# Kernel optimization log

Measured on AMD Instinct MI355X. Metric: run time of the kernel, lower is better.

## Reference

```python
import jax, jax.numpy as jnp
import numpy as np

B, L, D = 2, 2048, 2048
NH, NKV = 16, 8
HD = D // NH            # 128
GQ = NH // NKV          # queries per kv head
THETA = 10000.0
SCALE = HD ** -0.5


def rope_tables(seq_len, dim, theta):
    inv_freq = 1.0 / theta ** (jnp.arange(0, dim, 2, dtype=jnp.float32) / dim)
    t = jnp.arange(seq_len, dtype=jnp.float32)
    freqs = jnp.outer(t, inv_freq)              # [L, dim/2]
    emb = jnp.concatenate([freqs, freqs], -1)   # [L, dim]
    return jnp.cos(emb), jnp.sin(emb)


def rotate_half(x):
    x1, x2 = jnp.split(x, 2, axis=-1)
    return jnp.concatenate([-x2, x1], -1)


def setup_inputs() -> dict:
    key = jax.random.key(0)
    ks = jax.random.split(key, 5)
    s = 0.02
    return {
        "x": jax.random.normal(ks[0], (B, L, D), jnp.float32),
        "Wq": jax.random.normal(ks[1], (NH * HD, D), jnp.float32) * s,
        "Wk": jax.random.normal(ks[2], (NKV * HD, D), jnp.float32) * s,
        "Wv": jax.random.normal(ks[3], (NKV * HD, D), jnp.float32) * s,
        "Wo": jax.random.normal(ks[4], (D, D), jnp.float32) * s,
    }


def reference(x, Wq, Wk, Wv, Wo):
    b, l, d = x.shape
    q = (x @ Wq.T).reshape(b, l, NH, HD).transpose(0, 2, 1, 3)    # [B,NH,L,HD]
    k = (x @ Wk.T).reshape(b, l, NKV, HD).transpose(0, 2, 1, 3)   # [B,NKV,L,HD]
    v = (x @ Wv.T).reshape(b, l, NKV, HD).transpose(0, 2, 1, 3)

    cos, sin = rope_tables(l, HD, THETA)                           # [L,HD]
    q = q * cos + rotate_half(q) * sin
    k = k * cos + rotate_half(k) * sin

    # GQA without materializing expanded K/V: group queries per kv head
    qg = q.reshape(b, NKV, GQ, l, HD)
    scores = jnp.einsum('bgrld,bgmd->bgrlm', qg, k) * SCALE        # [B,NKV,GQ,L,L]
    causal = jnp.triu(jnp.ones((l, l), bool), k=1)
    scores = jnp.where(causal, -jnp.inf, scores)
    attn = jax.nn.softmax(scores.astype(jnp.float32), axis=-1).astype(q.dtype)
    out = jnp.einsum('bgrlm,bgmd->bgrld', attn, v)                 # [B,NKV,GQ,L,HD]
    out = out.reshape(b, NH, l, HD).transpose(0, 2, 1, 3).reshape(b, l, d)
    return out @ Wo.T
```

## Files before the change

kernel.cpp:

```cpp
#include <hip/hip_runtime.h>
#include <cmath>

using u16 = unsigned short;
typedef u16    u16x4  __attribute__((ext_vector_type(4)));
typedef u16    u16x8  __attribute__((ext_vector_type(8)));
typedef __bf16 bf16x8 __attribute__((ext_vector_type(8)));
typedef float  f32x4  __attribute__((ext_vector_type(4)));

constexpr int Bc  = 2;
constexpr int Lc  = 2048;
constexpr int Dc  = 2048;
constexpr int NHc = 16;
constexpr int NKVc= 8;
constexpr int HDc = 128;

__device__ __forceinline__ u16 f2b(float f) {
  union { float f; unsigned u; } v; v.f = f;
  unsigned r = v.u + 0x7FFFu + ((v.u >> 16) & 1u);
  return (u16)(r >> 16);
}
__device__ __forceinline__ u16 f2b_fast(float f) {
  union { float f; unsigned u; } v; v.f = f;
  return (u16)((v.u + 0x8000u) >> 16);
}
__device__ __forceinline__ float b2f(u16 s) {
  union { unsigned u; float f; } v; v.u = ((unsigned)s) << 16;
  return v.f;
}
__device__ __forceinline__ bf16x8 ld_frag(const u16* p) {
  u16x8 u = *(const u16x8*)p;
  return __builtin_bit_cast(bf16x8, u);
}
__device__ __forceinline__ void gld_lds16(u16* ldst, const u16* gsrc) {
  __builtin_amdgcn_global_load_lds(
      (const __attribute__((address_space(1))) void*)gsrc,
      (__attribute__((address_space(3))) void*)ldst, 16, 0, 0);
}

__global__ void cvt_f32_bf16(const float* __restrict__ src, u16* __restrict__ dst, int n) {
  int i = (blockIdx.x * blockDim.x + threadIdx.x) * 4;
  if (i >= n) return;
  float4 v = *(const float4*)&src[i];
  u16x4 o = { f2b(v.x), f2b(v.y), f2b(v.z), f2b(v.w) };
  *(u16x4*)&dst[i] = o;
}

template <int MODE>
__global__ __launch_bounds__(256) void gemm_lds(
    const u16* __restrict__ A, const u16* __restrict__ W,
    float* __restrict__ Cf, u16* __restrict__ Qp, u16* __restrict__ Kp, u16* __restrict__ Vtp,
    int M, int N, int K)
{
  __shared__ u16 lds[16384];
  u16* lA = lds;
  u16* lB = lds + 8192;
  const int tid  = threadIdx.x;
  const int wave = tid >> 6, lane = tid & 63;
  const int quad = lane >> 4, l16 = lane & 15;
  const int t7   = l16 & 7;
  const int m0 = blockIdx.y * 128, n0 = blockIdx.x * 128;
  const int mw = (wave >> 1) * 64, nw = (wave & 1) * 64;
  const int r8 = lane >> 3;
  const int cgl = (lane & 7) ^ r8;

  f32x4 acc[4][4];
#pragma unroll
  for (int i = 0; i < 4; ++i)
#pragma unroll
    for (int j = 0; j < 4; ++j) acc[i][j] = {0.f, 0.f, 0.f, 0.f};

  for (int kt = 0; kt < K; kt += 64) {
#pragma unroll
    for (int cc = 0; cc < 4; ++cc) {
      int c = wave + cc * 4;
      gld_lds16(&lA[c * 512], &A[(size_t)(m0 + 8 * c + r8) * K + kt + cgl * 8]);
      gld_lds16(&lB[c * 512], &W[(size_t)(n0 + 8 * c + r8) * K + kt + cgl * 8]);
    }
    __syncthreads();
#pragma unroll
    for (int s = 0; s < 2; ++s) {
      bf16x8 af[4], bf[4];
#pragma unroll
      for (int i = 0; i < 4; ++i)
        af[i] = ld_frag(&lA[(mw + i*16 + l16) * 64 + ((quad + 4*s) ^ t7) * 8]);
#pragma unroll
      for (int j = 0; j < 4; ++j)
        bf[j] = ld_frag(&lB[(nw + j*16 + l16) * 64 + ((quad + 4*s) ^ t7) * 8]);
#pragma unroll
      for (int i = 0; i < 4; ++i)
#pragma unroll
        for (int j = 0; j < 4; ++j)
          acc[i][j] = __builtin_amdgcn_mfma_f32_16x16x32_bf16(af[i], bf[j], acc[i][j], 0, 0, 0);
    }
    __syncthreads();
  }

  if constexpr (MODE == 1) {
#pragma unroll
    for (int i = 0; i < 4; ++i)
#pragma unroll
      for (int j = 0; j < 4; ++j)
#pragma unroll
        for (int r = 0; r < 4; ++r) {
          int m = m0 + mw + i*16 + quad*4 + r;
          int n = n0 + nw + j*16 + l16;
          Cf[(size_t)m * N + n] = acc[i][j][r];
        }
  } else {
    if (n0 < 3072) {
      u16* Cb; int ldc, nc0;
      if (n0 < 2048) { Cb = Qp; ldc = 2048; nc0 = n0; }
      else           { Cb = Kp; ldc = 1024; nc0 = n0 - 2048; }
#pragma unroll
      for (int i = 0; i < 4; ++i)
#pragma unroll
        for (int j = 0; j < 4; ++j)
#pragma unroll
          for (int r = 0; r < 4; ++r) {
            int m = m0 + mw + i*16 + quad*4 + r;
            int n = nc0 + nw + j*16 + l16;
            Cb[(size_t)m * ldc + n] = f2b(acc[i][j][r]);
          }
    } else {
#pragma unroll
      for (int i = 0; i < 4; ++i)
#pragma unroll
        for (int j = 0; j < 4; ++j)
#pragma unroll
          for (int r = 0; r < 4; ++r) {
            int l = mw + i*16 + quad*4 + r;
            int d = nw + j*16 + l16;
            int dp = d ^ (((l >> 3) & 15) << 3);
            lds[l * 128 + dp] = f2b(acc[i][j][r]);
          }
      __syncthreads();
      const int b   = m0 >> 11;
      const int hkv = (n0 - 3072) >> 7;
      const size_t vbase = (((size_t)b * NKVc + hkv) * HDc) * (size_t)Lc;
#pragma unroll
      for (int it = 0; it < 8; ++it) {
        int slot = tid + it * 256;
        int d  = slot & 127;
        int l8 = slot >> 7;
        u16x8 v;
#pragma unroll
        for (int e = 0; e < 8; ++e) {
          int l = l8 * 8 + e;
          v[e] = lds[l * 128 + (d ^ (((l >> 3) & 15) << 3))];
        }
        *(u16x8*)&Vtp[vbase + (size_t)d * Lc + (m0 & (Lc - 1)) + l8 * 8] = v;
      }
    }
  }
}

__global__ void rope_kernel(u16* __restrict__ T, int nheads, float oscale)
{
  int idx = blockIdx.x * blockDim.x + threadIdx.x;
  int total = Bc * Lc * nheads * 64;
  if (idx >= total) return;
  int d   = idx & 63;
  int h   = (idx >> 6) % nheads;
  int row = idx / (nheads * 64);
  int l   = row & (Lc - 1);
  float freq = exp2f((float)d * (-13.287712379549449f / 64.f));
  float ang  = (float)l * freq;
  float s, c;
  sincosf(ang, &s, &c);
  size_t base = (size_t)row * (nheads * 128) + h * 128;
  float x1 = b2f(T[base + d]);
  float x2 = b2f(T[base + d + 64]);
  T[base + d]      = f2b((x1 * c - x2 * s) * oscale);
  T[base + d + 64] = f2b((x2 * c + x1 * s) * oscale);
}

__global__ __launch_bounds__(256) void flash_kernel(
    const u16* __restrict__ Q, const u16* __restrict__ K, const u16* __restrict__ Vt,
    u16* __restrict__ O)
{
  __shared__ u16 smem[37376];
  const int tid  = threadIdx.x;
  const int wave = tid >> 6, lane = tid & 63;
  const int quad = lane >> 4, l16 = lane & 15;
  const int bh = blockIdx.x;
  const int b = bh >> 4, h = bh & 15, hkv = h >> 1;

  const size_t kbase = ((size_t)b * Lc) * (NKVc * HDc) + (size_t)hkv * HDc;
  const size_t vbase = (((size_t)b * NKVc + hkv) * HDc) * (size_t)Lc;

  const int kr8  = lane >> 4;
  const int kcl  = lane & 15;
  const int vr16 = lane >> 3;
  const int vkl  = lane & 7;

  u16* sP_w = smem + 32768 + wave * 1152;

  for (int pass = 0; pass < 2; ++pass) {
    const int qt = (pass == 0) ? (31 - (int)blockIdx.y) : (int)blockIdx.y;
    const int q0 = qt * 64;
    const size_t qbase = ((size_t)(b * Lc + q0)) * Dc + (size_t)h * HDc;

    __syncthreads();
    {
      u16* sQ = smem + 24576;
#pragma unroll
      for (int i = 0; i < 4; ++i) {
        int g = tid + i * 256;
        int row = g >> 4, cg = g & 15;
        *(u16x8*)&sQ[row * 128 + (cg ^ (row & 15)) * 8] =
            *(const u16x8*)&Q[qbase + (size_t)row * Dc + cg * 8];
      }
      __syncthreads();
      bf16x8 qf0 = ld_frag(&sQ[(wave*16 + l16) * 128 + ((0*4 + quad) ^ l16) * 8]);
      bf16x8 qf1 = ld_frag(&sQ[(wave*16 + l16) * 128 + ((1*4 + quad) ^ l16) * 8]);
      bf16x8 qf2 = ld_frag(&sQ[(wave*16 + l16) * 128 + ((2*4 + quad) ^ l16) * 8]);
      bf16x8 qf3 = ld_frag(&sQ[(wave*16 + l16) * 128 + ((3*4 + quad) ^ l16) * 8]);
      bf16x8 qf[4] = { qf0, qf1, qf2, qf3 };

#pragma unroll
      for (int cc = 0; cc < 4; ++cc) {
        int c = wave + cc * 4;
        int row = c * 4 + kr8;
        gld_lds16(smem + c * 512,
                  &K[kbase + (size_t)row * (NKVc*HDc) + (size_t)(kcl ^ (row & 15)) * 8]);
      }
#pragma unroll
      for (int cc = 0; cc < 4; ++cc) {
        int c = wave + cc * 4;
        int d = c * 8 + vr16;
        gld_lds16(smem + 16384 + c * 512,
                  &Vt[vbase + (size_t)d * Lc + (size_t)(vkl ^ (d & 7)) * 8]);
      }

      f32x4 acc_o[8];
#pragma unroll
      for (int i = 0; i < 8; ++i) acc_o[i] = {0.f, 0.f, 0.f, 0.f};
      float ps[4] = {0.f, 0.f, 0.f, 0.f};

      for (int kt = 0; kt <= qt; ++kt) {
        const int kOff  = (kt & 1) ? 8192 : 0;
        const int kOffN = (kt & 1) ? 0 : 8192;
        const int vOff  = 16384 + ((kt & 1) ? 8192 : 0);
        const int vOffN = 16384 + ((kt & 1) ? 0 : 8192);

        __asm__ volatile("s_waitcnt vmcnt(4)\n\ts_barrier" ::: "memory");

        if (kt < qt) {
#pragma unroll
          for (int cc = 0; cc < 4; ++cc) {
            int c = wave + cc * 4;
            int row = (kt + 1) * 64 + c * 4 + kr8;
            gld_lds16(smem + kOffN + c * 512,
                      &K[kbase + (size_t)row * (NKVc*HDc) + (size_t)(kcl ^ (row & 15)) * 8]);
          }
        }

        const u16* sKc = smem + kOff;
        f32x4 accs[4];
#pragma unroll
        for (int n = 0; n < 4; ++n) accs[n] = {0.f, 0.f, 0.f, 0.f};
#pragma unroll
        for (int ks = 0; ks < 4; ++ks)
#pragma unroll
          for (int n = 0; n < 4; ++n) {
            bf16x8 kf = ld_frag(&sKc[(n*16 + l16) * 128 + ((ks*4 + quad) ^ l16) * 8]);
            accs[n] = __builtin_amdgcn_mfma_f32_16x16x32_bf16(qf[ks], kf, accs[n], 0, 0, 0);
          }

        const int qrow = q0 + wave*16 + quad*4;
        if (kt == qt) {
#pragma unroll
          for (int n = 0; n < 4; ++n) {
            int kg = kt*64 + n*16 + l16;
#pragma unroll
            for (int r = 0; r < 4; ++r)
              if (kg > qrow + r) accs[n][r] = -INFINITY;
          }
        }
#pragma unroll
        for (int n = 0; n < 4; ++n)
#pragma unroll
          for (int r = 0; r < 4; ++r) {
            float p = exp2f(accs[n][r]);
            accs[n][r] = p;
            ps[r] += p;
          }

#pragma unroll
        for (int n = 0; n < 4; ++n)
#pragma unroll
          for (int r = 0; r < 4; ++r)
            sP_w[(quad*4 + r) * 72 + n*16 + l16] = f2b_fast(accs[n][r]);

        if (kt < qt)
          __asm__ volatile("s_waitcnt vmcnt(4) lgkmcnt(0)\n\ts_barrier" ::: "memory");
        else
          __asm__ volatile("s_waitcnt vmcnt(0) lgkmcnt(0)\n\ts_barrier" ::: "memory");

        if (kt < qt) {
#pragma unroll
          for (int cc = 0; cc < 4; ++cc) {
            int c = wave + cc * 4;
            int d = c * 8 + vr16;
            gld_lds16(smem + vOffN + c * 512,
                      &Vt[vbase + (size_t)d * Lc + (kt+1)*64 + (size_t)(vkl ^ (d & 7)) * 8]);
          }
        }

        const u16* sVc = smem + vOff;
#pragma unroll
        for (int s2 = 0; s2 < 2; ++s2) {
          bf16x8 pf = ld_frag(&sP_w[l16 * 72 + s2*32 + quad*8]);
#pragma unroll
          for (int di = 0; di < 8; ++di) {
            bf16x8 vf = ld_frag(&sVc[(di*16 + l16) * 64 + ((s2*4 + quad) ^ (l16 & 7)) * 8]);
            acc_o[di] = __builtin_amdgcn_mfma_f32_16x16x32_bf16(pf, vf, acc_o[di], 0, 0, 0);
          }
        }
      }

#pragma unroll
      for (int off = 1; off < 16; off <<= 1)
#pragma unroll
        for (int r = 0; r < 4; ++r) ps[r] += __shfl_xor(ps[r], off);
      float inv[4];
#pragma unroll
      for (int r = 0; r < 4; ++r) inv[r] = 1.0f / ps[r];

#pragma unroll
      for (int di = 0; di < 8; ++di)
#pragma unroll
        for (int r = 0; r < 4; ++r) {
          int qrow = q0 + wave*16 + quad*4 + r;
          int d = di*16 + l16;
          float v = acc_o[di][r] * inv[r];
          O[((size_t)(b * Lc + qrow)) * Dc + (size_t)h * HDc + d] = f2b(v);
        }
    }
  }
}

extern "C" void kernel_launch(void* const* d_in, const int* in_sizes, int n_in,
                              void* d_out, int out_size, void* d_ws, size_t ws_size,
                              hipStream_t stream)
{
  const float* x  = (const float*)d_in[0];
  const float* Wq = (const float*)d_in[1];
  const float* Wk = (const float*)d_in[2];
  const float* Wv = (const float*)d_in[3];
  const float* Wo = (const float*)d_in[4];
  float* out = (float*)d_out;

  const int M = Bc * Lc;
  u16* ws = (u16*)d_ws;
  u16* xb   = ws;
  u16* Ow   = xb;
  u16* Wcat = ws + (size_t)8 * 1024 * 1024;
  u16* Wob  = Wcat;
  u16* Qw   = Wcat + (size_t)8 * 1024 * 1024;
  u16* Kw   = Qw   + (size_t)8 * 1024 * 1024;
  u16* Vt   = Kw   + (size_t)4 * 1024 * 1024;

  const int nx = M * Dc;
  const int nq = Dc * Dc;
  const int nk = (NKVc*HDc) * Dc;
  cvt_f32_bf16<<<nx/1024, 256, 0, stream>>>(x,  xb, nx);
  cvt_f32_bf16<<<nq/1024, 256, 0, stream>>>(Wq, Wcat, nq);
  cvt_f32_bf16<<<nk/1024, 256, 0, stream>>>(Wk, Wcat + (size_t)2048*2048, nk);
  cvt_f32_bf16<<<nk/1024, 256, 0, stream>>>(Wv, Wcat + (size_t)3072*2048, nk);

  gemm_lds<2><<<dim3(32, 32), 256, 0, stream>>>(xb, Wcat, nullptr, Qw, Kw, Vt, M, 4096, Dc);

  const float qs = 0.08838834764831845f * 1.4426950408889634f;
  rope_kernel<<<(M * NHc  * 64 + 255) / 256, 256, 0, stream>>>(Qw, NHc,  qs);
  rope_kernel<<<(M * NKVc * 64 + 255) / 256, 256, 0, stream>>>(Kw, NKVc, 1.0f);

  flash_kernel<<<dim3(Bc*NHc, 16), 256, 0, stream>>>(Qw, Kw, Vt, Ow);

  cvt_f32_bf16<<<nq/1024, 256, 0, stream>>>(Wo, Wob, nq);
  gemm_lds<1><<<dim3(16, 32), 256, 0, stream>>>(Ow, Wob, out, nullptr, nullptr, nullptr, M, Dc, Dc);
}
```

Baseline: 345.5 us.

## Share K/V tiles across GQA query heads in flash kernel, merge small launches

The flash kernel now launches one 512-thread block per (batch, kv head) and processes both query heads of that GQA group together. Each K/V tile is loaded into LDS once and used by 8 waves instead of 4, which halves K/V global traffic and the number of blocks. The three weight conversions are merged into one kernel, and the two RoPE launches into one, to cut launch overhead. The trade-offs are fewer blocks in flight (256 instead of 512), a larger LDS footprint, and barriers that now synchronise 8 waves.

```diff
diff --git a/kernel.cpp b/kernel.cpp
--- a/kernel.cpp
+++ b/kernel.cpp
@@ -41,6 +41,22 @@
   int i = (blockIdx.x * blockDim.x + threadIdx.x) * 4;
   if (i >= n) return;
   float4 v = *(const float4*)&src[i];
+  u16x4 o = { f2b(v.x), f2b(v.y), f2b(v.z), f2b(v.w) };
+  *(u16x4*)&dst[i] = o;
+}
+
+__global__ void cvt_w3(const float* __restrict__ Wq, const float* __restrict__ Wk,
+                       const float* __restrict__ Wv, u16* __restrict__ dst) {
+  const int n1 = Dc * Dc;
+  const int n2 = n1 + (NKVc*HDc) * Dc;
+  const int n3 = n2 + (NKVc*HDc) * Dc;
+  int i = (blockIdx.x * blockDim.x + threadIdx.x) * 4;
+  if (i >= n3) return;
+  const float* src; int off;
+  if (i < n1)      { src = Wq; off = i; }
+  else if (i < n2) { src = Wk; off = i - n1; }
+  else             { src = Wv; off = i - n2; }
+  float4 v = *(const float4*)&src[off];
   u16x4 o = { f2b(v.x), f2b(v.y), f2b(v.z), f2b(v.w) };
   *(u16x4*)&dst[i] = o;
 }
@@ -154,11 +170,15 @@
   }
 }
 
-__global__ void rope_kernel(u16* __restrict__ T, int nheads, float oscale)
+__global__ void rope2_kernel(u16* __restrict__ Qp, u16* __restrict__ Kp, float qs)
 {
-  int idx = blockIdx.x * blockDim.x + threadIdx.x;
-  int total = Bc * Lc * nheads * 64;
-  if (idx >= total) return;
+  const int nQ = Bc * Lc * NHc * 64;
+  const int nT = nQ + Bc * Lc * NKVc * 64;
+  int t = blockIdx.x * blockDim.x + threadIdx.x;
+  if (t >= nT) return;
+  u16* T; int nheads; float osc; int idx;
+  if (t < nQ) { T = Qp; nheads = NHc;  osc = qs;  idx = t; }
+  else        { T = Kp; nheads = NKVc; osc = 1.f; idx = t - nQ; }
   int d   = idx & 63;
   int h   = (idx >> 6) % nheads;
   int row = idx / (nheads * 64);
@@ -170,26 +190,28 @@
   size_t base = (size_t)row * (nheads * 128) + h * 128;
   float x1 = b2f(T[base + d]);
   float x2 = b2f(T[base + d + 64]);
-  T[base + d]      = f2b((x1 * c - x2 * s) * oscale);
-  T[base + d + 64] = f2b((x2 * c + x1 * s) * oscale);
-}
-
-__global__ __launch_bounds__(256) void flash_kernel(
+  T[base + d]      = f2b((x1 * c - x2 * s) * osc);
+  T[base + d + 64] = f2b((x2 * c + x1 * s) * osc);
+}
+
+__global__ __launch_bounds__(512) void flash_kernel(
     const u16* __restrict__ Q, const u16* __restrict__ K, const u16* __restrict__ Vt,
     u16* __restrict__ O)
 {
-  __shared__ u16 smem[37376];
+  __shared__ u16 smem[41984];
   const int tid  = threadIdx.x;
   const int wave = tid >> 6, lane = tid & 63;
   const int quad = lane >> 4, l16 = lane & 15;
-  const int bh = blockIdx.x;
-  const int b = bh >> 4, h = bh & 15, hkv = h >> 1;
+  const int hw = wave >> 2, wr = wave & 3;
+  const int bhkv = blockIdx.x;
+  const int b = bhkv >> 3, hkv = bhkv & 7;
+  const int h = hkv * 2 + hw;
 
   const size_t kbase = ((size_t)b * Lc) * (NKVc * HDc) + (size_t)hkv * HDc;
   const size_t vbase = (((size_t)b * NKVc + hkv) * HDc) * (size_t)Lc;
 
-  const int kr8  = lane >> 4;
-  const int kcl  = lane & 15;
+  const int kr8 = lane >> 4;
+  const int kcl = lane & 15;
   const int vr16 = lane >> 3;
   const int vkl  = lane & 7;
 
@@ -198,145 +220,143 @@
   for (int pass = 0; pass < 2; ++pass) {
     const int qt = (pass == 0) ? (31 - (int)blockIdx.y) : (int)blockIdx.y;
     const int q0 = qt * 64;
-    const size_t qbase = ((size_t)(b * Lc + q0)) * Dc + (size_t)h * HDc;
 
     __syncthreads();
-    {
-      u16* sQ = smem + 24576;
-#pragma unroll
-      for (int i = 0; i < 4; ++i) {
-        int g = tid + i * 256;
-        int row = g >> 4, cg = g & 15;
-        *(u16x8*)&sQ[row * 128 + (cg ^ (row & 15)) * 8] =
-            *(const u16x8*)&Q[qbase + (size_t)row * Dc + cg * 8];
-      }
-      __syncthreads();
-      bf16x8 qf0 = ld_frag(&sQ[(wave*16 + l16) * 128 + ((0*4 + quad) ^ l16) * 8]);
-      bf16x8 qf1 = ld_frag(&sQ[(wave*16 + l16) * 128 + ((1*4 + quad) ^ l16) * 8]);
-      bf16x8 qf2 = ld_frag(&sQ[(wave*16 + l16) * 128 + ((2*4 + quad) ^ l16) * 8]);
-      bf16x8 qf3 = ld_frag(&sQ[(wave*16 + l16) * 128 + ((3*4 + quad) ^ l16) * 8]);
-      bf16x8 qf[4] = { qf0, qf1, qf2, qf3 };
-
-#pragma unroll
-      for (int cc = 0; cc < 4; ++cc) {
-        int c = wave + cc * 4;
-        int row = c * 4 + kr8;
-        gld_lds16(smem + c * 512,
-                  &K[kbase + (size_t)row * (NKVc*HDc) + (size_t)(kcl ^ (row & 15)) * 8]);
-      }
-#pragma unroll
-      for (int cc = 0; cc < 4; ++cc) {
-        int c = wave + cc * 4;
-        int d = c * 8 + vr16;
-        gld_lds16(smem + 16384 + c * 512,
-                  &Vt[vbase + (size_t)d * Lc + (size_t)(vkl ^ (d & 7)) * 8]);
-      }
-
-      f32x4 acc_o[8];
-#pragma unroll
-      for (int i = 0; i < 8; ++i) acc_o[i] = {0.f, 0.f, 0.f, 0.f};
-      float ps[4] = {0.f, 0.f, 0.f, 0.f};
-
-      for (int kt = 0; kt <= qt; ++kt) {
-        const int kOff  = (kt & 1) ? 8192 : 0;
-        const int kOffN = (kt & 1) ? 0 : 8192;
-        const int vOff  = 16384 + ((kt & 1) ? 8192 : 0);
-        const int vOffN = 16384 + ((kt & 1) ? 0 : 8192);
-
-        __asm__ volatile("s_waitcnt vmcnt(4)\n\ts_barrier" ::: "memory");
-
-        if (kt < qt) {
-#pragma unroll
-          for (int cc = 0; cc < 4; ++cc) {
-            int c = wave + cc * 4;
-            int row = (kt + 1) * 64 + c * 4 + kr8;
-            gld_lds16(smem + kOffN + c * 512,
-                      &K[kbase + (size_t)row * (NKVc*HDc) + (size_t)(kcl ^ (row & 15)) * 8]);
-          }
-        }
-
-        const u16* sKc = smem + kOff;
-        f32x4 accs[4];
-#pragma unroll
-        for (int n = 0; n < 4; ++n) accs[n] = {0.f, 0.f, 0.f, 0.f};
-#pragma unroll
-        for (int ks = 0; ks < 4; ++ks)
-#pragma unroll
-          for (int n = 0; n < 4; ++n) {
-            bf16x8 kf = ld_frag(&sKc[(n*16 + l16) * 128 + ((ks*4 + quad) ^ l16) * 8]);
-            accs[n] = __builtin_amdgcn_mfma_f32_16x16x32_bf16(qf[ks], kf, accs[n], 0, 0, 0);
-          }
-
-        const int qrow = q0 + wave*16 + quad*4;
-        if (kt == qt) {
-#pragma unroll
-          for (int n = 0; n < 4; ++n) {
-            int kg = kt*64 + n*16 + l16;
-#pragma unroll
-            for (int r = 0; r < 4; ++r)
-              if (kg > qrow + r) accs[n][r] = -INFINITY;
-          }
-        }
-#pragma unroll
-        for (int n = 0; n < 4; ++n)
-#pragma unroll
-          for (int r = 0; r < 4; ++r) {
-            float p = exp2f(accs[n][r]);
-            accs[n][r] = p;
-            ps[r] += p;
-          }
-
-#pragma unroll
-        for (int n = 0; n < 4; ++n)
+#pragma unroll
+    for (int i = 0; i < 4; ++i) {
+      int g = tid + i * 512;
+      int row = g >> 4, cg = g & 15;
+      int qh = hkv * 2 + (row >> 6);
+      int rr = row & 63;
+      *(u16x8*)&smem[row * 128 + (cg ^ (row & 15)) * 8] =
+          *(const u16x8*)&Q[((size_t)(b * Lc + q0 + rr)) * Dc + (size_t)qh * HDc + cg * 8];
+    }
+    __syncthreads();
+    bf16x8 qf[4];
+#pragma unroll
+    for (int ks = 0; ks < 4; ++ks)
+      qf[ks] = ld_frag(&smem[(hw*64 + wr*16 + l16) * 128 + ((ks*4 + quad) ^ l16) * 8]);
+    __syncthreads();
+
+#pragma unroll
+    for (int i = 0; i < 2; ++i) {
+      int c = wave + i * 8;
+      int row = c * 4 + kr8;
+      gld_lds16(smem + c * 512,
+                &K[kbase + (size_t)row * (NKVc*HDc) + (size_t)(kcl ^ (row & 15)) * 8]);
+    }
+#pragma unroll
+    for (int i = 0; i < 2; ++i) {
+      int c = wave + i * 8;
+      int d = c * 8 + vr16;
+      gld_lds16(smem + 16384 + c * 512,
+                &Vt[vbase + (size_t)d * Lc + (size_t)(vkl ^ (d & 7)) * 8]);
+    }
+
+    f32x4 acc_o[8];
+#pragma unroll
+    for (int i = 0; i < 8; ++i) acc_o[i] = {0.f, 0.f, 0.f, 0.f};
+    float ps[4] = {0.f, 0.f, 0.f, 0.f};
+
+    for (int kt = 0; kt <= qt; ++kt) {
+      const int kOff  = (kt & 1) ? 8192 : 0;
+      const int kOffN = (kt & 1) ? 0 : 8192;
+      const int vOff  = (kt & 1) ? 24576 : 16384;
+      const int vOffN = (kt & 1) ? 16384 : 24576;
+
+      __asm__ volatile("s_waitcnt vmcnt(2)\n\ts_barrier" ::: "memory");
+
+      if (kt < qt) {
+#pragma unroll
+        for (int i = 0; i < 2; ++i) {
+          int c = wave + i * 8;
+          int row = (kt + 1) * 64 + c * 4 + kr8;
+          gld_lds16(smem + kOffN + c * 512,
+                    &K[kbase + (size_t)row * (NKVc*HDc) + (size_t)(kcl ^ (row & 15)) * 8]);
+        }
+      }
+
+      const u16* sKc = smem + kOff;
+      f32x4 accs[4];
+#pragma unroll
+      for (int n = 0; n < 4; ++n) accs[n] = {0.f, 0.f, 0.f, 0.f};
+#pragma unroll
+      for (int ks = 0; ks < 4; ++ks)
+#pragma unroll
+        for (int n = 0; n < 4; ++n) {
+          bf16x8 kf = ld_frag(&sKc[(n*16 + l16) * 128 + ((ks*4 + quad) ^ l16) * 8]);
+          accs[n] = __builtin_amdgcn_mfma_f32_16x16x32_bf16(qf[ks], kf, accs[n], 0, 0, 0);
+        }
+
+      const int qrow = q0 + wr*16 + quad*4;
+      if (kt == qt) {
+#pragma unroll
+        for (int n = 0; n < 4; ++n) {
+          int kg = kt*64 + n*16 + l16;
 #pragma unroll
           for (int r = 0; r < 4; ++r)
-            sP_w[(quad*4 + r) * 72 + n*16 + l16] = f2b_fast(accs[n][r]);
-
-        if (kt < qt)
-          __asm__ volatile("s_waitcnt vmcnt(4) lgkmcnt(0)\n\ts_barrier" ::: "memory");
-        else
-          __asm__ volatile("s_waitcnt vmcnt(0) lgkmcnt(0)\n\ts_barrier" ::: "memory");
-
-        if (kt < qt) {
-#pragma unroll
-          for (int cc = 0; cc < 4; ++cc) {
-            int c = wave + cc * 4;
-            int d = c * 8 + vr16;
-            gld_lds16(smem + vOffN + c * 512,
-                      &Vt[vbase + (size_t)d * Lc + (kt+1)*64 + (size_t)(vkl ^ (d & 7)) * 8]);
-          }
-        }
-
-        const u16* sVc = smem + vOff;
-#pragma unroll
-        for (int s2 = 0; s2 < 2; ++s2) {
-          bf16x8 pf = ld_frag(&sP_w[l16 * 72 + s2*32 + quad*8]);
-#pragma unroll
-          for (int di = 0; di < 8; ++di) {
-            bf16x8 vf = ld_frag(&sVc[(di*16 + l16) * 64 + ((s2*4 + quad) ^ (l16 & 7)) * 8]);
-            acc_o[di] = __builtin_amdgcn_mfma_f32_16x16x32_bf16(pf, vf, acc_o[di], 0, 0, 0);
-          }
-        }
-      }
-
-#pragma unroll
-      for (int off = 1; off < 16; off <<= 1)
-#pragma unroll
-        for (int r = 0; r < 4; ++r) ps[r] += __shfl_xor(ps[r], off);
-      float inv[4];
-#pragma unroll
-      for (int r = 0; r < 4; ++r) inv[r] = 1.0f / ps[r];
-
-#pragma unroll
-      for (int di = 0; di < 8; ++di)
+            if (kg > qrow + r) accs[n][r] = -INFINITY;
+        }
+      }
+#pragma unroll
+      for (int n = 0; n < 4; ++n)
 #pragma unroll
         for (int r = 0; r < 4; ++r) {
-          int qrow = q0 + wave*16 + quad*4 + r;
-          int d = di*16 + l16;
-          float v = acc_o[di][r] * inv[r];
-          O[((size_t)(b * Lc + qrow)) * Dc + (size_t)h * HDc + d] = f2b(v);
-        }
-    }
+          float p = exp2f(accs[n][r]);
+          accs[n][r] = p;
+          ps[r] += p;
+        }
+
+#pragma unroll
+      for (int n = 0; n < 4; ++n)
+#pragma unroll
+        for (int r = 0; r < 4; ++r)
+          sP_w[(quad*4 + r) * 72 + n*16 + l16] = f2b_fast(accs[n][r]);
+
+      if (kt < qt)
+        __asm__ volatile("s_waitcnt vmcnt(2) lgkmcnt(0)\n\ts_barrier" ::: "memory");
+      else
+        __asm__ volatile("s_waitcnt vmcnt(0) lgkmcnt(0)\n\ts_barrier" ::: "memory");
+
+      if (kt < qt) {
+#pragma unroll
+        for (int i = 0; i < 2; ++i) {
+          int c = wave + i * 8;
+          int d = c * 8 + vr16;
+          gld_lds16(smem + vOffN + c * 512,
+                    &Vt[vbase + (size_t)d * Lc + (kt+1)*64 + (size_t)(vkl ^ (d & 7)) * 8]);
+        }
+      }
+
+      const u16* sVc = smem + vOff;
+#pragma unroll
+      for (int s2 = 0; s2 < 2; ++s2) {
+        bf16x8 pf = ld_frag(&sP_w[l16 * 72 + s2*32 + quad*8]);
+#pragma unroll
+        for (int di = 0; di < 8; ++di) {
+          bf16x8 vf = ld_frag(&sVc[(di*16 + l16) * 64 + ((s2*4 + quad) ^ (l16 & 7)) * 8]);
+          acc_o[di] = __builtin_amdgcn_mfma_f32_16x16x32_bf16(pf, vf, acc_o[di], 0, 0, 0);
+        }
+      }
+    }
+
+#pragma unroll
+    for (int off = 1; off < 16; off <<= 1)
+#pragma unroll
+      for (int r = 0; r < 4; ++r) ps[r] += __shfl_xor(ps[r], off);
+    float inv[4];
+#pragma unroll
+    for (int r = 0; r < 4; ++r) inv[r] = 1.0f / ps[r];
+
+#pragma unroll
+    for (int di = 0; di < 8; ++di)
+#pragma unroll
+      for (int r = 0; r < 4; ++r) {
+        int qrow = q0 + wr*16 + quad*4 + r;
+        int d = di*16 + l16;
+        float v = acc_o[di][r] * inv[r];
+        O[((size_t)(b * Lc + qrow)) * Dc + (size_t)h * HDc + d] = f2b(v);
+      }
   }
 }
 
@@ -363,19 +383,17 @@
 
   const int nx = M * Dc;
   const int nq = Dc * Dc;
-  const int nk = (NKVc*HDc) * Dc;
-  cvt_f32_bf16<<<nx/1024, 256, 0, stream>>>(x,  xb, nx);
-  cvt_f32_bf16<<<nq/1024, 256, 0, stream>>>(Wq, Wcat, nq);
-  cvt_f32_bf16<<<nk/1024, 256, 0, stream>>>(Wk, Wcat + (size_t)2048*2048, nk);
-  cvt_f32_bf16<<<nk/1024, 256, 0, stream>>>(Wv, Wcat + (size_t)3072*2048, nk);
+  const int nw3 = nq + 2 * (NKVc*HDc) * Dc;
+  cvt_f32_bf16<<<nx/1024, 256, 0, stream>>>(x, xb, nx);
+  cvt_w3<<<nw3/1024, 256, 0, stream>>>(Wq, Wk, Wv, Wcat);
 
   gemm_lds<2><<<dim3(32, 32), 256, 0, stream>>>(xb, Wcat, nullptr, Qw, Kw, Vt, M, 4096, Dc);
 
   const float qs = 0.08838834764831845f * 1.4426950408889634f;
-  rope_kernel<<<(M * NHc  * 64 + 255) / 256, 256, 0, stream>>>(Qw, NHc,  qs);
-  rope_kernel<<<(M * NKVc * 64 + 255) / 256, 256, 0, stream>>>(Kw, NKVc, 1.0f);
-
-  flash_kernel<<<dim3(Bc*NHc, 16), 256, 0, stream>>>(Qw, Kw, Vt, Ow);
+  const int nrope = M * (NHc + NKVc) * 64;
+  rope2_kernel<<<(nrope + 255) / 256, 256, 0, stream>>>(Qw, Kw, qs);
+
+  flash_kernel<<<dim3(Bc*NKVc, 16), 512, 0, stream>>>(Qw, Kw, Vt, Ow);
 
   cvt_f32_bf16<<<nq/1024, 256, 0, stream>>>(Wo, Wob, nq);
   gemm_lds<1><<<dim3(16, 32), 256, 0, stream>>>(Ow, Wob, out, nullptr, nullptr, nullptr, M, Dc, Dc);
```

Result: faster. 331.2 us (-4.1%).
